# Kernel tuning notes

Measured on AMD Instinct MI355X. Metric: run time of the kernel, lower is better.

The kernel has to match this reference:

```python
import jax, jax.numpy as jnp
import numpy as np

NUM_EMBEDDINGS = 4096
EMBEDDING_DIM = 64
COMMITMENT_COST = 0.25
DECAY = 0.99
EPSILON = 1e-05


def setup_inputs() -> dict:
    key = jax.random.key(0)
    k1, k2, k3, k4 = jax.random.split(key, 4)
    z = jax.random.normal(k1, (128, 24, 1536), dtype=jnp.float32)
    embedding = jax.random.normal(k2, (NUM_EMBEDDINGS, EMBEDDING_DIM), dtype=jnp.float32) * 0.05
    ema_cluster_size = jax.random.uniform(k3, (NUM_EMBEDDINGS,), dtype=jnp.float32)
    ema_w = jax.random.normal(k4, (NUM_EMBEDDINGS, EMBEDDING_DIM), dtype=jnp.float32) * 0.05
    return {"z": z, "embedding": embedding, "ema_cluster_size": ema_cluster_size, "ema_w": ema_w}


def reference(z, embedding, ema_cluster_size, ema_w):
    # VectorQuantizer.forward in training mode (EMA codebook update).
    K, d = embedding.shape
    B = z.shape[0]
    z_flat = z.reshape(-1, d)  # [N, d], N = B*576

    # Pairwise squared distances: ||z||^2 + ||e||^2 - 2 z e^T  -> [N, K]
    dist = (jnp.sum(z_flat * z_flat, axis=1, keepdims=True)
            + jnp.sum(embedding * embedding, axis=1)
            - 2.0 * (z_flat @ embedding.T))
    codes = jnp.argmin(dist, axis=1)  # [N]

    # EMA statistics (one-hot scatter expressed as segment sums)
    counts = jax.ops.segment_sum(jnp.ones_like(codes, dtype=z.dtype), codes, num_segments=K)
    new_cluster_size = DECAY * ema_cluster_size + (1.0 - DECAY) * counts
    dw = jax.ops.segment_sum(z_flat, codes, num_segments=K)  # [K, d]
    new_ema_w = DECAY * ema_w + (1.0 - DECAY) * dw

    n = jnp.sum(new_cluster_size)
    cluster_size = (new_cluster_size + EPSILON) / (n + K * EPSILON) * n
    new_embedding = new_ema_w / cluster_size[:, None]

    # Quantize with the UPDATED codebook (torch copies weights before embedding lookup)
    z_q = new_embedding[codes].reshape(z.shape)
    vq_loss = COMMITMENT_COST * jnp.mean((jax.lax.stop_gradient(z_q) - z) ** 2)
    z_q_st = z + jax.lax.stop_gradient(z_q - z)  # straight-through
    codes = codes.reshape(B, -1)  # [B, 576]
    return (vq_loss, z_q_st, codes, new_embedding, new_cluster_size, new_ema_w)
```

## Files before the change

### kernel.cpp

```cpp
#include <hip/hip_runtime.h>

constexpr int KC    = 4096;
constexpr int DIM   = 64;
constexpr int NROWS = 73728;
constexpr int NELEM = 4718592;

typedef _Float16 f16x8 __attribute__((ext_vector_type(8)));
typedef float    f32x4 __attribute__((ext_vector_type(4)));

constexpr size_t OUT_LOSS  = 0;
constexpr size_t OUT_ZQ    = 1;
constexpr size_t OUT_CODES = 1 + (size_t)NELEM;
constexpr size_t OUT_EMB   = OUT_CODES + (size_t)NROWS;
constexpr size_t OUT_NCS   = OUT_EMB + (size_t)KC * DIM;
constexpr size_t OUT_NEW   = OUT_NCS + (size_t)KC;

constexpr size_t alignup(size_t x, size_t a) { return (x + a - 1) & ~(a - 1); }
constexpr size_t WS_CODES  = 0;
constexpr size_t WS_COUNTS = WS_CODES + sizeof(int) * (size_t)NROWS;
constexpr size_t WS_OFFS   = WS_COUNTS + sizeof(int) * (size_t)KC;
constexpr size_t WS_CURSOR = alignup(WS_OFFS + sizeof(int) * (KC + 1), 16);
constexpr size_t WS_SORTED = WS_CURSOR + sizeof(int) * (size_t)KC;
constexpr size_t WS_E2     = alignup(WS_SORTED + sizeof(int) * (size_t)NROWS, 16);
constexpr size_t WS_N      = WS_E2 + sizeof(float) * (size_t)KC;
constexpr size_t WS_LOSSD  = alignup(WS_N + sizeof(float), 8);
constexpr size_t WS_EMBPK  = alignup(WS_LOSSD + 8, 16);

__global__ void k_prep(const float* __restrict__ emb, char* __restrict__ emb_pk,
                       float* __restrict__ e2s, int* __restrict__ counts) {
    if (threadIdx.x < 32) counts[blockIdx.x * 32 + threadIdx.x] = 0;
    int t = blockIdx.x * 256 + threadIdx.x;
    int c = t >> 3, q = t & 7;
    const float* ep = emb + (size_t)c * DIM + q * 8;
    f16x8 hv, lv;
    float s = 0.f;
    #pragma unroll
    for (int e = 0; e < 8; ++e) {
        float x = ep[e];
        _Float16 h = (_Float16)x;
        float r = x - (float)h;
        hv[e] = h;
        lv[e] = (_Float16)(r * 2048.0f);
        s = fmaf(x, x, s);
    }
    s += __shfl_xor(s, 1, 64);
    s += __shfl_xor(s, 2, 64);
    s += __shfl_xor(s, 4, 64);
    if (q == 0) e2s[c] = 1024.0f * s;
    int g = c >> 4, lc = c & 15;
    int h = q >> 2, lq = q & 3;
    int lane = lq * 16 + lc;
    char* base = emb_pk + (size_t)g * 4096 + lane * 16;
    *(f16x8*)(base + h * 1024)       = hv;
    *(f16x8*)(base + (2 + h) * 1024) = lv;
}

__global__ __launch_bounds__(192, 3) void k_argmin5(
        const float* __restrict__ z, const char* __restrict__ emb_pk,
        const float* __restrict__ e2s,
        int* __restrict__ codes_i, float* __restrict__ codes_f,
        int* __restrict__ counts) {
    __shared__ int codebuf[3][32];

    const int tid = threadIdx.x;
    const int l   = tid & 63;
    const int w   = tid >> 6;
    const int lc  = l & 15;
    const int lq  = l >> 4;
    const int waveRow = blockIdx.x * 96 + w * 32;

    f16x8 ah2k[2][2], ahr[2][2], al2k[2][2];
    #pragma unroll
    for (int rt = 0; rt < 2; ++rt)
        #pragma unroll
        for (int h = 0; h < 2; ++h) {
            const float* zp = z + (size_t)(waveRow + rt * 16 + lc) * DIM + h * 32 + lq * 8;
            float4 x0 = *(const float4*)zp;
            float4 x1 = *(const float4*)(zp + 4);
            float xs[8] = {x0.x, x0.y, x0.z, x0.w, x1.x, x1.y, x1.z, x1.w};
            #pragma unroll
            for (int e = 0; e < 8; ++e) {
                _Float16 hh = (_Float16)xs[e];
                float rr = xs[e] - (float)hh;
                ahr[rt][h][e]  = -hh;
                ah2k[rt][h][e] = (_Float16)(-2048.0f * (float)hh);
                al2k[rt][h][e] = -(_Float16)(rr * 2048.0f);
            }
        }

    float best[2][4];
    int   bestk[2][4];
    #pragma unroll
    for (int rt = 0; rt < 2; ++rt)
        #pragma unroll
        for (int j = 0; j < 4; ++j) { best[rt][j] = INFINITY; bestk[rt][j] = 0; }

    const char* pk = emb_pk + l * 16;

#define LOADG(EC, B0, B1, B2, B3, G) {                                   \
        const char* p_ = pk + (size_t)(G) * 4096;                        \
        B0 = *(const f16x8*)(p_);                                        \
        B1 = *(const f16x8*)(p_ + 1024);                                 \
        B2 = *(const f16x8*)(p_ + 2048);                                 \
        B3 = *(const f16x8*)(p_ + 3072);                                 \
        EC = e2s[(G) * 16 + lc]; }

#define COMPUTE(B0, B1, B2, B3, EC, G) {                                          \
        _Pragma("unroll")                                                         \
        for (int rt = 0; rt < 2; ++rt) {                                          \
            f32x4 acc; acc[0] = EC; acc[1] = EC; acc[2] = EC; acc[3] = EC;        \
            acc = __builtin_amdgcn_mfma_f32_16x16x32_f16(ah2k[rt][0], B0, acc, 0, 0, 0); \
            acc = __builtin_amdgcn_mfma_f32_16x16x32_f16(ah2k[rt][1], B1, acc, 0, 0, 0); \
            acc = __builtin_amdgcn_mfma_f32_16x16x32_f16(ahr[rt][0],  B2, acc, 0, 0, 0); \
            acc = __builtin_amdgcn_mfma_f32_16x16x32_f16(ahr[rt][1],  B3, acc, 0, 0, 0); \
            acc = __builtin_amdgcn_mfma_f32_16x16x32_f16(al2k[rt][0], B0, acc, 0, 0, 0); \
            acc = __builtin_amdgcn_mfma_f32_16x16x32_f16(al2k[rt][1], B1, acc, 0, 0, 0); \
            _Pragma("unroll")                                                     \
            for (int j = 0; j < 4; ++j) {                                         \
                if (acc[j] < best[rt][j]) { best[rt][j] = acc[j]; bestk[rt][j] = (G) * 16 + lc; } \
            }                                                                     \
        } }

    {
        f16x8 A0, A1, A2, A3, B0, B1, B2, B3, C0, C1, C2, C3, D0, D1, D2, D3;
        float eA, eB, eC, eD;
        LOADG(eA, A0, A1, A2, A3, 0);
        LOADG(eB, B0, B1, B2, B3, 1);
        LOADG(eC, C0, C1, C2, C3, 2);
        for (int g = 0; g < 252; g += 4) {
            LOADG(eD, D0, D1, D2, D3, g + 3);
            COMPUTE(A0, A1, A2, A3, eA, g);
            LOADG(eA, A0, A1, A2, A3, g + 4);
            COMPUTE(B0, B1, B2, B3, eB, g + 1);
            LOADG(eB, B0, B1, B2, B3, g + 5);
            COMPUTE(C0, C1, C2, C3, eC, g + 2);
            LOADG(eC, C0, C1, C2, C3, g + 6);
            COMPUTE(D0, D1, D2, D3, eD, g + 3);
        }
        LOADG(eD, D0, D1, D2, D3, 255);
        COMPUTE(A0, A1, A2, A3, eA, 252);
        COMPUTE(B0, B1, B2, B3, eB, 253);
        COMPUTE(C0, C1, C2, C3, eC, 254);
        COMPUTE(D0, D1, D2, D3, eD, 255);
    }
#undef LOADG
#undef COMPUTE

    #pragma unroll
    for (int rt = 0; rt < 2; ++rt)
        #pragma unroll
        for (int j = 0; j < 4; ++j) {
            float b = best[rt][j];
            int   k = bestk[rt][j];
            #pragma unroll
            for (int m = 1; m < 16; m <<= 1) {
                float obv = __shfl_xor(b, m, 64);
                int   okv = __shfl_xor(k, m, 64);
                if (obv < b || (obv == b && okv < k)) { b = obv; k = okv; }
            }
            if (lc == 0) codebuf[w][rt * 16 + lq * 4 + j] = k;
        }

    if (l < 32) {
        int code = codebuf[w][l];
        size_t rowg = (size_t)waveRow + l;
        codes_i[rowg] = code;
        codes_f[rowg] = (float)code;
        atomicAdd(&counts[code], 1);
    }
}

__global__ void k_scan(const int* __restrict__ counts,
                       int* __restrict__ offsets, int* __restrict__ cursor,
                       const float* __restrict__ ema_cs, float* __restrict__ ncs_out,
                       float* __restrict__ n_out, double* __restrict__ lossp) {
    __shared__ int   part[256];
    __shared__ float fpart[256];
    int tid = threadIdx.x;
    if (tid == 0) *lossp = 0.0;
    int base = tid * 16;
    int loc[16];
    int s = 0;
    float fs = 0.f;
    #pragma unroll
    for (int j = 0; j < 16; ++j) {
        int cnt = counts[base + j];
        loc[j] = s; s += cnt;
        float v = 0.99f * ema_cs[base + j] + 0.01f * (float)cnt;
        ncs_out[base + j] = v;
        fs += v;
    }
    part[tid] = s;
    fpart[tid] = fs;
    __syncthreads();
    for (int off = 1; off < 256; off <<= 1) {
        int v = (tid >= off) ? part[tid - off] : 0;
        __syncthreads();
        part[tid] += v;
        __syncthreads();
    }
    int excl = part[tid] - s;
    #pragma unroll
    for (int j = 0; j < 16; ++j) {
        int o = excl + loc[j];
        offsets[base + j] = o;
        cursor[base + j]  = o;
    }
    if (tid == 255) offsets[KC] = excl + s;
    for (int m = 128; m > 0; m >>= 1) {
        if (tid < m) fpart[tid] += fpart[tid + m];
        __syncthreads();
    }
    if (tid == 0) n_out[0] = fpart[0];
}

__global__ void k_scatteridx(const int* __restrict__ codes_i,
                             int* __restrict__ cursor, int* __restrict__ sorted_rows) {
    int r = blockIdx.x * 256 + threadIdx.x;
    if (r < NROWS) {
        int c = codes_i[r];
        int p = atomicAdd(&cursor[c], 1);
        sorted_rows[p] = r;
    }
}

__global__ __launch_bounds__(64) void k_dwsum(
        const float* __restrict__ z, const int* __restrict__ offsets,
        const int* __restrict__ sorted_rows, const float* __restrict__ ema_w,
        const float* __restrict__ ncs, const float* __restrict__ nptr,
        float* __restrict__ new_ema_w_out, float* __restrict__ new_emb_out) {
    int k = blockIdx.x, tid = threadIdx.x;
    int beg = offsets[k], end = offsets[k + 1];
    float a0 = 0.f, a1 = 0.f, a2 = 0.f, a3 = 0.f;
    int i = beg;
    for (; i + 3 < end; i += 4) {
        int r0 = sorted_rows[i], r1 = sorted_rows[i + 1];
        int r2 = sorted_rows[i + 2], r3 = sorted_rows[i + 3];
        a0 += z[(size_t)r0 * DIM + tid];
        a1 += z[(size_t)r1 * DIM + tid];
        a2 += z[(size_t)r2 * DIM + tid];
        a3 += z[(size_t)r3 * DIM + tid];
    }
    for (; i < end; ++i) a0 += z[(size_t)sorted_rows[i] * DIM + tid];
    float dwv = (a0 + a1) + (a2 + a3);
    size_t idx = (size_t)k * DIM + tid;
    float n = nptr[0];
    float nw = 0.99f * ema_w[idx] + 0.01f * dwv;
    float cs = (ncs[k] + 1e-5f) / (n + 4096.0f * 1e-5f) * n;
    new_ema_w_out[idx] = nw;
    new_emb_out[idx] = nw / cs;
}

__global__ __launch_bounds__(256) void k_quant(
        const float* __restrict__ z, const float* __restrict__ new_emb,
        const int* __restrict__ codes, float* __restrict__ zq_out,
        double* __restrict__ loss_acc) {
    __shared__ double red[256];
    const int nvec = NELEM / 4;
    int t = blockIdx.x * 256 + threadIdx.x;
    int stride = gridDim.x * 256;
    double ls = 0.0;
    for (int v = t; v < nvec; v += stride) {
        int e0 = v * 4;
        int n  = e0 >> 6;
        int d0 = e0 & 63;
        int code = codes[n];
        float4 zq = *(const float4*)&new_emb[(size_t)code * DIM + d0];
        float4 zv = *(const float4*)&z[e0];
        float dx = zq.x - zv.x, dy = zq.y - zv.y, dz = zq.z - zv.z, dw4 = zq.w - zv.w;
        float4 o;
        o.x = zv.x + dx; o.y = zv.y + dy; o.z = zv.z + dz; o.w = zv.w + dw4;
        *(float4*)&zq_out[e0] = o;
        ls += (double)(dx * dx) + (double)(dy * dy) + (double)(dz * dz) + (double)(dw4 * dw4);
    }
    red[threadIdx.x] = ls;
    __syncthreads();
    for (int m = 128; m > 0; m >>= 1) {
        if (threadIdx.x < m) red[threadIdx.x] += red[threadIdx.x + m];
        __syncthreads();
    }
    if (threadIdx.x == 0) atomicAdd(loss_acc, red[0]);
}

__global__ void k_loss(const double* __restrict__ loss_acc, float* __restrict__ out0) {
    out0[0] = (float)(0.25 * (loss_acc[0] / (double)NELEM));
}

extern "C" void kernel_launch(void* const* d_in, const int* in_sizes, int n_in,
                              void* d_out, int out_size, void* d_ws, size_t ws_size,
                              hipStream_t stream) {
    const float* z      = (const float*)d_in[0];
    const float* emb    = (const float*)d_in[1];
    const float* ema_cs = (const float*)d_in[2];
    const float* ema_w  = (const float*)d_in[3];
    float* out = (float*)d_out;
    char*  ws  = (char*)d_ws;

    int*    codes_i = (int*)(ws + WS_CODES);
    int*    counts  = (int*)(ws + WS_COUNTS);
    int*    offsets = (int*)(ws + WS_OFFS);
    int*    cursor  = (int*)(ws + WS_CURSOR);
    int*    sorted  = (int*)(ws + WS_SORTED);
    float*  e2s     = (float*)(ws + WS_E2);
    float*  nptr    = (float*)(ws + WS_N);
    double* lossp   = (double*)(ws + WS_LOSSD);
    char*   emb_pk  = ws + WS_EMBPK;

    k_prep<<<(KC * 8) / 256, 256, 0, stream>>>(emb, emb_pk, e2s, counts);
    k_argmin5<<<NROWS / 96, 192, 0, stream>>>(z, emb_pk, e2s, codes_i,
                                              out + OUT_CODES, counts);
    k_scan<<<1, 256, 0, stream>>>(counts, offsets, cursor, ema_cs,
                                  out + OUT_NCS, nptr, lossp);
    k_scatteridx<<<(NROWS + 255) / 256, 256, 0, stream>>>(codes_i, cursor, sorted);
    k_dwsum<<<KC, 64, 0, stream>>>(z, offsets, sorted, ema_w,
                                   out + OUT_NCS, nptr, out + OUT_NEW, out + OUT_EMB);
    k_quant<<<1152, 256, 0, stream>>>(z, out + OUT_EMB, codes_i,
                                      out + OUT_ZQ, lossp);
    k_loss<<<1, 1, 0, stream>>>(lossp, out + OUT_LOSS);
}
```

Before: 186.5 us.

## Interleave codebook norms into packed groups and hand-pipeline argmin loads with asm

Stores each codebook group's squared norms alongside its packed fp16 tiles so a group is one contiguous block. The argmin kernel issues those loads with inline-asm global loads and explicit vmcnt waits, keeping four groups in flight. It tracks the best group index instead of the full code to save instructions. It bypasses the compiler's memory scheduling and over-fetches past the last group, relying on workspace slack.

```diff
diff --git a/kernel.cpp b/kernel.cpp
--- a/kernel.cpp
+++ b/kernel.cpp
@@ -4,6 +4,7 @@
 constexpr int DIM   = 64;
 constexpr int NROWS = 73728;
 constexpr int NELEM = 4718592;
+constexpr int GSTRIDE = 4160;
 
 typedef _Float16 f16x8 __attribute__((ext_vector_type(8)));
 typedef float    f32x4 __attribute__((ext_vector_type(4)));
@@ -21,13 +22,12 @@
 constexpr size_t WS_OFFS   = WS_COUNTS + sizeof(int) * (size_t)KC;
 constexpr size_t WS_CURSOR = alignup(WS_OFFS + sizeof(int) * (KC + 1), 16);
 constexpr size_t WS_SORTED = WS_CURSOR + sizeof(int) * (size_t)KC;
-constexpr size_t WS_E2     = alignup(WS_SORTED + sizeof(int) * (size_t)NROWS, 16);
-constexpr size_t WS_N      = WS_E2 + sizeof(float) * (size_t)KC;
+constexpr size_t WS_N      = alignup(WS_SORTED + sizeof(int) * (size_t)NROWS, 16);
 constexpr size_t WS_LOSSD  = alignup(WS_N + sizeof(float), 8);
-constexpr size_t WS_EMBPK  = alignup(WS_LOSSD + 8, 16);
+constexpr size_t WS_EMBPK  = alignup(WS_LOSSD + 8, 64);
 
 __global__ void k_prep(const float* __restrict__ emb, char* __restrict__ emb_pk,
-                       float* __restrict__ e2s, int* __restrict__ counts) {
+                       int* __restrict__ counts) {
     if (threadIdx.x < 32) counts[blockIdx.x * 32 + threadIdx.x] = 0;
     int t = blockIdx.x * 256 + threadIdx.x;
     int c = t >> 3, q = t & 7;
@@ -46,18 +46,18 @@
     s += __shfl_xor(s, 1, 64);
     s += __shfl_xor(s, 2, 64);
     s += __shfl_xor(s, 4, 64);
-    if (q == 0) e2s[c] = 1024.0f * s;
     int g = c >> 4, lc = c & 15;
     int h = q >> 2, lq = q & 3;
     int lane = lq * 16 + lc;
-    char* base = emb_pk + (size_t)g * 4096 + lane * 16;
+    char* gbase = emb_pk + (size_t)g * GSTRIDE;
+    if (q == 0) *(float*)(gbase + lc * 4) = 1024.0f * s;
+    char* base = gbase + 64 + lane * 16;
     *(f16x8*)(base + h * 1024)       = hv;
     *(f16x8*)(base + (2 + h) * 1024) = lv;
 }
 
-__global__ __launch_bounds__(192, 3) void k_argmin5(
+__global__ __launch_bounds__(192, 3) void k_argmin6(
         const float* __restrict__ z, const char* __restrict__ emb_pk,
-        const float* __restrict__ e2s,
         int* __restrict__ codes_i, float* __restrict__ codes_f,
         int* __restrict__ counts) {
     __shared__ int codebuf[3][32];
@@ -89,69 +89,72 @@
         }
 
     float best[2][4];
-    int   bestk[2][4];
+    int   bestg[2][4];
     #pragma unroll
     for (int rt = 0; rt < 2; ++rt)
         #pragma unroll
-        for (int j = 0; j < 4; ++j) { best[rt][j] = INFINITY; bestk[rt][j] = 0; }
-
-    const char* pk = emb_pk + l * 16;
-
-#define LOADG(EC, B0, B1, B2, B3, G) {                                   \
-        const char* p_ = pk + (size_t)(G) * 4096;                        \
-        B0 = *(const f16x8*)(p_);                                        \
-        B1 = *(const f16x8*)(p_ + 1024);                                 \
-        B2 = *(const f16x8*)(p_ + 2048);                                 \
-        B3 = *(const f16x8*)(p_ + 3072);                                 \
-        EC = e2s[(G) * 16 + lc]; }
-
-#define COMPUTE(B0, B1, B2, B3, EC, G) {                                          \
+        for (int j = 0; j < 4; ++j) { best[rt][j] = INFINITY; bestg[rt][j] = 0; }
+
+    const unsigned long long pkb = (unsigned long long)emb_pk;
+    unsigned voffA = 64 + l * 16;
+    unsigned voffB = lc * 4;
+
+    f16x8 b00, b01, b02, b03, b10, b11, b12, b13;
+    f16x8 b20, b21, b22, b23, b30, b31, b32, b33;
+    float e0, e1, e2v, e3;
+
+#define ISSUE(B0, B1, B2, B3, EV)                                                        \
+    asm volatile("global_load_dword %0, %1, %2"             : "=v"(EV) : "v"(voffB), "s"(pkb)); \
+    asm volatile("global_load_dwordx4 %0, %1, %2"             : "=v"(B0) : "v"(voffA), "s"(pkb)); \
+    asm volatile("global_load_dwordx4 %0, %1, %2 offset:1024" : "=v"(B1) : "v"(voffA), "s"(pkb)); \
+    asm volatile("global_load_dwordx4 %0, %1, %2 offset:2048" : "=v"(B2) : "v"(voffA), "s"(pkb)); \
+    asm volatile("global_load_dwordx4 %0, %1, %2 offset:3072" : "=v"(B3) : "v"(voffA), "s"(pkb)); \
+    voffA += GSTRIDE; voffB += GSTRIDE;
+
+#define WAITP                                                \
+    asm volatile("s_waitcnt vmcnt(15)" ::: "memory");        \
+    __builtin_amdgcn_sched_barrier(0);
+
+#define COMP(B0, B1, B2, B3, EV, G) {                                             \
+        f32x4 ci; ci[0] = EV; ci[1] = EV; ci[2] = EV; ci[3] = EV;                 \
         _Pragma("unroll")                                                         \
         for (int rt = 0; rt < 2; ++rt) {                                          \
-            f32x4 acc; acc[0] = EC; acc[1] = EC; acc[2] = EC; acc[3] = EC;        \
-            acc = __builtin_amdgcn_mfma_f32_16x16x32_f16(ah2k[rt][0], B0, acc, 0, 0, 0); \
-            acc = __builtin_amdgcn_mfma_f32_16x16x32_f16(ah2k[rt][1], B1, acc, 0, 0, 0); \
-            acc = __builtin_amdgcn_mfma_f32_16x16x32_f16(ahr[rt][0],  B2, acc, 0, 0, 0); \
-            acc = __builtin_amdgcn_mfma_f32_16x16x32_f16(ahr[rt][1],  B3, acc, 0, 0, 0); \
-            acc = __builtin_amdgcn_mfma_f32_16x16x32_f16(al2k[rt][0], B0, acc, 0, 0, 0); \
-            acc = __builtin_amdgcn_mfma_f32_16x16x32_f16(al2k[rt][1], B1, acc, 0, 0, 0); \
+            f32x4 acc = __builtin_amdgcn_mfma_f32_16x16x32_f16(ah2k[rt][0], B0, ci, 0, 0, 0); \
+            acc = __builtin_amdgcn_mfma_f32_16x16x32_f16(ah2k[rt][1], B1, acc, 0, 0, 0);      \
+            acc = __builtin_amdgcn_mfma_f32_16x16x32_f16(ahr[rt][0],  B2, acc, 0, 0, 0);      \
+            acc = __builtin_amdgcn_mfma_f32_16x16x32_f16(ahr[rt][1],  B3, acc, 0, 0, 0);      \
+            acc = __builtin_amdgcn_mfma_f32_16x16x32_f16(al2k[rt][0], B0, acc, 0, 0, 0);      \
+            acc = __builtin_amdgcn_mfma_f32_16x16x32_f16(al2k[rt][1], B1, acc, 0, 0, 0);      \
             _Pragma("unroll")                                                     \
             for (int j = 0; j < 4; ++j) {                                         \
-                if (acc[j] < best[rt][j]) { best[rt][j] = acc[j]; bestk[rt][j] = (G) * 16 + lc; } \
+                if (acc[j] < best[rt][j]) { best[rt][j] = acc[j]; bestg[rt][j] = (G); } \
             }                                                                     \
         } }
 
-    {
-        f16x8 A0, A1, A2, A3, B0, B1, B2, B3, C0, C1, C2, C3, D0, D1, D2, D3;
-        float eA, eB, eC, eD;
-        LOADG(eA, A0, A1, A2, A3, 0);
-        LOADG(eB, B0, B1, B2, B3, 1);
-        LOADG(eC, C0, C1, C2, C3, 2);
-        for (int g = 0; g < 252; g += 4) {
-            LOADG(eD, D0, D1, D2, D3, g + 3);
-            COMPUTE(A0, A1, A2, A3, eA, g);
-            LOADG(eA, A0, A1, A2, A3, g + 4);
-            COMPUTE(B0, B1, B2, B3, eB, g + 1);
-            LOADG(eB, B0, B1, B2, B3, g + 5);
-            COMPUTE(C0, C1, C2, C3, eC, g + 2);
-            LOADG(eC, C0, C1, C2, C3, g + 6);
-            COMPUTE(D0, D1, D2, D3, eD, g + 3);
-        }
-        LOADG(eD, D0, D1, D2, D3, 255);
-        COMPUTE(A0, A1, A2, A3, eA, 252);
-        COMPUTE(B0, B1, B2, B3, eB, 253);
-        COMPUTE(C0, C1, C2, C3, eC, 254);
-        COMPUTE(D0, D1, D2, D3, eD, 255);
-    }
-#undef LOADG
-#undef COMPUTE
+    __builtin_amdgcn_sched_barrier(0);
+    ISSUE(b00, b01, b02, b03, e0)
+    ISSUE(b10, b11, b12, b13, e1)
+    ISSUE(b20, b21, b22, b23, e2v)
+    ISSUE(b30, b31, b32, b33, e3)
+
+    for (int g = 0; g < 256; g += 4) {
+        WAITP  COMP(b00, b01, b02, b03, e0,  g)      ISSUE(b00, b01, b02, b03, e0)
+        WAITP  COMP(b10, b11, b12, b13, e1,  g + 1)  ISSUE(b10, b11, b12, b13, e1)
+        WAITP  COMP(b20, b21, b22, b23, e2v, g + 2)  ISSUE(b20, b21, b22, b23, e2v)
+        WAITP  COMP(b30, b31, b32, b33, e3,  g + 3)  ISSUE(b30, b31, b32, b33, e3)
+    }
+    asm volatile("s_waitcnt vmcnt(0)" ::: "memory");
+    __builtin_amdgcn_sched_barrier(0);
+#undef ISSUE
+#undef WAITP
+#undef COMP
 
     #pragma unroll
     for (int rt = 0; rt < 2; ++rt)
         #pragma unroll
         for (int j = 0; j < 4; ++j) {
             float b = best[rt][j];
-            int   k = bestk[rt][j];
+            int   k = bestg[rt][j] * 16 + lc;
             #pragma unroll
             for (int m = 1; m < 16; m <<= 1) {
                 float obv = __shfl_xor(b, m, 64);
@@ -301,13 +304,14 @@
     int*    offsets = (int*)(ws + WS_OFFS);
     int*    cursor  = (int*)(ws + WS_CURSOR);
     int*    sorted  = (int*)(ws + WS_SORTED);
-    float*  e2s     = (float*)(ws + WS_E2);
     float*  nptr    = (float*)(ws + WS_N);
     double* lossp   = (double*)(ws + WS_LOSSD);
     char*   emb_pk  = ws + WS_EMBPK;
-
-    k_prep<<<(KC * 8) / 256, 256, 0, stream>>>(emb, emb_pk, e2s, counts);
-    k_argmin5<<<NROWS / 96, 192, 0, stream>>>(z, emb_pk, e2s, codes_i,
+    float*  dw      = nullptr;
+
+    (void)dw;
+    k_prep<<<(KC * 8) / 256, 256, 0, stream>>>(emb, emb_pk, counts);
+    k_argmin6<<<NROWS / 96, 192, 0, stream>>>(z, emb_pk, codes_i,
                                               out + OUT_CODES, counts);
     k_scan<<<1, 256, 0, stream>>>(counts, offsets, cursor, ema_cs,
                                   out + OUT_NCS, nptr, lossp);
```

Measured after the change: 180.4 us. 3.3% less time.
